# Performance work log

Hardware: AMD Instinct MI355X
Metric: run time of the kernel (lower is better)

## Reference

```python
import math
import jax, jax.numpy as jnp
import numpy as np

B, N, TOKEN_DIM = 8, 8192, 512
NODE_DIM = 64
MAX_NODES = 64
SCORE_HIDDEN = 64


def setup_inputs() -> dict:
    key = jax.random.key(0)
    ks = jax.random.split(key, 8)
    s = lambda k, shape, fan_in: jax.random.normal(k, shape, jnp.float32) / np.sqrt(fan_in)
    return {
        "token_feats": jax.random.normal(ks[0], (B, N, TOKEN_DIM), jnp.float32),
        "score_w1": s(ks[1], (TOKEN_DIM, SCORE_HIDDEN), TOKEN_DIM),
        "score_b1": jnp.zeros((SCORE_HIDDEN,), jnp.float32),
        "score_w2": s(ks[2], (SCORE_HIDDEN, 1), SCORE_HIDDEN),
        "score_b2": jnp.zeros((1,), jnp.float32),
        "t2n_w": s(ks[3], (TOKEN_DIM, NODE_DIM), TOKEN_DIM),
        "n2t_w": s(ks[4], (NODE_DIM, TOKEN_DIM), NODE_DIM),
        "gcn_w1": s(ks[5], (NODE_DIM, NODE_DIM), NODE_DIM),
        "gcn_w2": s(ks[6], (NODE_DIM, NODE_DIM), NODE_DIM),
    }


def reference(token_feats, score_w1, score_b1, score_w2, score_b2,
              t2n_w, n2t_w, gcn_w1, gcn_w2):
    Bn, Nn, d = token_feats.shape
    M = MAX_NODES
    eps = 1e-6

    # --- node selection (scores -> threshold -> top-k among selected) ---
    h = jax.nn.relu(jnp.einsum('bnd,dh->bnh', token_feats, score_w1) + score_b1)
    scores = (jnp.einsum('bnh,ho->bno', h, score_w2) + score_b2)[..., 0]  # [B,N]
    mean = scores.mean(axis=1, keepdims=True)
    std = scores.std(axis=1, keepdims=True)  # unbiased=False (population)
    thr = mean + 0.5 * std
    count = jnp.sum(scores > thr, axis=1)  # [B]
    fallback_k = min(M, max(4, Nn // 16))
    take_k = jnp.where(count == 0, fallback_k, jnp.minimum(count, M))  # [B]

    _, top_idx = jax.lax.top_k(scores, M)  # [B,M] highest scores; set == torch's selection
    node_mask = jnp.arange(M)[None, :] < take_k[:, None]  # [B,M] bool
    maskf = node_mask.astype(token_feats.dtype)

    gathered = jnp.take_along_axis(token_feats, top_idx[..., None], axis=1)  # [B,M,d]
    H0 = jnp.einsum('bmd,dk->bmk', gathered, t2n_w) * maskf[..., None]  # [B,M,node_dim]

    # --- cosine-similarity adjacency, masked, self-loops, row-normalized ---
    nrm = jnp.maximum(jnp.linalg.norm(H0, axis=-1, keepdims=True), eps)
    Hn = H0 / nrm
    A = jax.nn.relu(jnp.einsum('bik,bjk->bij', Hn, Hn))
    A = A * (maskf[:, :, None] * maskf[:, None, :])
    A = A + jnp.eye(M, dtype=A.dtype)[None] * maskf[:, None, :]
    A = A / jnp.maximum(A.sum(axis=-1, keepdims=True), 1e-6)

    # --- two-layer GCN (no bias) ---
    x = jax.nn.relu(jnp.einsum('bij,bjk,kl->bil', A, H0, gcn_w1))
    Hg = jax.nn.relu(jnp.einsum('bij,bjk,kl->bil', A, x, gcn_w2))  # [B,M,node_dim]

    # --- attention scatter-back to tokens ---
    token_proj = jnp.einsum('bnd,dk->bnk', token_feats, t2n_w)  # [B,N,node_dim]
    logits = jnp.einsum('bnk,bmk->bnm', token_proj, Hg) / math.sqrt(NODE_DIM)
    attn = jax.nn.softmax(logits, axis=-1)
    injected = jnp.einsum('bnm,bmk->bnk', attn, Hg)
    back = jnp.einsum('bnk,kd->bnd', injected, n2t_w)
    return token_feats + back
```

## Files before the change

kernel.cpp:

```cpp
#include <hip/hip_runtime.h>
#include <hip/hip_bf16.h>

#define B_ 8
#define N_ 8192
#define D_ 512
#define M_ 64

typedef unsigned short u16;
typedef unsigned int u32;
typedef __attribute__((ext_vector_type(8))) short bf16x8;
typedef __attribute__((ext_vector_type(4))) float f32x4;

__device__ __forceinline__ u16 f2bf(float f) {
  u32 u = __float_as_uint(f);
  u += 0x7FFFu + ((u >> 16) & 1u);
  return (u16)(u >> 16);
}
__device__ __forceinline__ float bf2f(u16 h) {
  return __uint_as_float(((u32)h) << 16);
}

__device__ __forceinline__ int bfrag_idx(int kd, int c, int ncols16) {
  int sub = (kd >> 5) * ncols16 + (c >> 4);
  int lane = (c & 15) + 16 * ((kd & 15) >> 2);
  int e = (kd & 3) + 4 * ((kd >> 4) & 1);
  return sub * 512 + lane * 8 + e;
}

__device__ __forceinline__ int kslot(int ln, int e) {
  return (e & 3) + 4 * (ln >> 4) + 16 * (e >> 2);
}

__device__ __forceinline__ bf16x8 pack8(float4 v0, float4 v1) {
  bf16x8 a;
  a[0] = (short)f2bf(v0.x); a[1] = (short)f2bf(v0.y);
  a[2] = (short)f2bf(v0.z); a[3] = (short)f2bf(v0.w);
  a[4] = (short)f2bf(v1.x); a[5] = (short)f2bf(v1.y);
  a[6] = (short)f2bf(v1.z); a[7] = (short)f2bf(v1.w);
  return a;
}

__global__ __launch_bounds__(256) void k_prep(
    const float* __restrict__ t2n, const float* __restrict__ n2t,
    const float* __restrict__ W1, const float* __restrict__ g1,
    const float* __restrict__ g2,
    u16* __restrict__ t2nf, u16* __restrict__ n2tf,
    u16* __restrict__ W1h, u16* __restrict__ W1l,
    u16* __restrict__ g1f, u16* __restrict__ g2f)
{
  const int gid = blockIdx.x * 256 + threadIdx.x;
  const int stride = gridDim.x * 256;
  for (int s = gid; s < 512 * 64; s += stride) {
    const int k = s >> 6, c = s & 63;
    const int idx = bfrag_idx(k, c, 4);
    t2nf[idx] = f2bf(t2n[s]);
    const float w = W1[s];
    const u16 wh = f2bf(w);
    W1h[idx] = wh;
    W1l[idx] = f2bf(w - bf2f(wh));
  }
  for (int s = gid; s < 64 * 512; s += stride) {
    const int k = s >> 9, c = s & 511;
    n2tf[bfrag_idx(k, c, 32)] = f2bf(n2t[s]);
  }
  for (int s = gid; s < 4096; s += stride) {
    const int k = s >> 6, c = s & 63;
    g1f[bfrag_idx(k, c, 4)] = f2bf(g1[s]);
    g2f[bfrag_idx(k, c, 4)] = f2bf(g2[s]);
  }
}

__global__ __launch_bounds__(256, 4) void k_sp(
    const float* __restrict__ X, const u16* __restrict__ W1h,
    const u16* __restrict__ W1l, const u16* __restrict__ t2nf,
    const float* __restrict__ b1, const float* __restrict__ w2,
    const float* __restrict__ b2, float* __restrict__ scores,
    float* __restrict__ outStash)
{
  __shared__ __align__(16) u16 sB[6144];
  __shared__ __align__(16) u16 sAf[4096];
  const int tid = threadIdx.x;
  const int t0 = blockIdx.x * 64;
  const int wv = tid >> 6, ln = tid & 63;
  const int lq = ln >> 4, lr = ln & 15;
  u16* mySf = &sAf[wv * 1024];
  const float* xr = X + (size_t)(t0 + 16 * wv + lr) * D_;

  f32x4 acc[4], accP[4];
  #pragma unroll
  for (int cb = 0; cb < 4; ++cb) {
    acc[cb] = (f32x4){0.f, 0.f, 0.f, 0.f};
    accP[cb] = (f32x4){0.f, 0.f, 0.f, 0.f};
  }

  auto gsrc = [&](int f, int kb) -> const u16* {
    const int cb = f / 3, mat = f % 3;
    const u16* mp = (mat == 0) ? W1h : (mat == 1) ? W1l : t2nf;
    return mp + (kb * 4 + cb) * 512 + ln * 8;
  };

  bf16x8 wr[3];
  #pragma unroll
  for (int j = 0; j < 3; ++j) wr[j] = *(const bf16x8*)gsrc(j * 4 + wv, 0);
  float4 va0 = *(const float4*)(xr + 4 * lq);
  float4 va1 = *(const float4*)(xr + 16 + 4 * lq);

  for (int kb = 0; kb < 16; ++kb) {
    __syncthreads();
    #pragma unroll
    for (int j = 0; j < 3; ++j)
      *(bf16x8*)&sB[(j * 4 + wv) * 512 + ln * 8] = wr[j];
    __syncthreads();
    const float4 v0 = va0, v1 = va1;
    if (kb < 15) {
      #pragma unroll
      for (int j = 0; j < 3; ++j) wr[j] = *(const bf16x8*)gsrc(j * 4 + wv, kb + 1);
      va0 = *(const float4*)(xr + 32 * (kb + 1) + 4 * lq);
      va1 = *(const float4*)(xr + 32 * (kb + 1) + 16 + 4 * lq);
    }
    const float xs[8] = {v0.x, v0.y, v0.z, v0.w, v1.x, v1.y, v1.z, v1.w};
    bf16x8 ah, al;
    #pragma unroll
    for (int e = 0; e < 8; ++e) {
      const u16 h = f2bf(xs[e]);
      ah[e] = (short)h;
      al[e] = (short)f2bf(xs[e] - bf2f(h));
    }
    #pragma unroll
    for (int cb = 0; cb < 4; ++cb) {
      const bf16x8 bh = *(const bf16x8*)&sB[(cb * 3 + 0) * 512 + ln * 8];
      const bf16x8 bl = *(const bf16x8*)&sB[(cb * 3 + 1) * 512 + ln * 8];
      const bf16x8 bt = *(const bf16x8*)&sB[(cb * 3 + 2) * 512 + ln * 8];
      acc[cb]  = __builtin_amdgcn_mfma_f32_16x16x32_bf16(ah, bh, acc[cb], 0, 0, 0);
      acc[cb]  = __builtin_amdgcn_mfma_f32_16x16x32_bf16(ah, bl, acc[cb], 0, 0, 0);
      acc[cb]  = __builtin_amdgcn_mfma_f32_16x16x32_bf16(al, bh, acc[cb], 0, 0, 0);
      accP[cb] = __builtin_amdgcn_mfma_f32_16x16x32_bf16(ah, bt, accP[cb], 0, 0, 0);
    }
  }

  float b1v[4], w2v[4];
  #pragma unroll
  for (int cb = 0; cb < 4; ++cb) {
    const int col = cb * 16 + lr;
    b1v[cb] = b1[col]; w2v[cb] = w2[col];
  }
  const float b2v = b2[0];
  #pragma unroll
  for (int r = 0; r < 4; ++r) {
    float p = 0.f;
    #pragma unroll
    for (int cb = 0; cb < 4; ++cb) {
      const float h = fmaxf(acc[cb][r] + b1v[cb], 0.f);
      p = fmaf(h, w2v[cb], p);
    }
    p += __shfl_xor(p, 1); p += __shfl_xor(p, 2);
    p += __shfl_xor(p, 4); p += __shfl_xor(p, 8);
    if (lr == 0) scores[t0 + wv * 16 + 4 * lq + r] = p + b2v;
  }

  #pragma unroll
  for (int cb = 0; cb < 4; ++cb)
    #pragma unroll
    for (int r = 0; r < 4; ++r) {
      const int idx = (cb >> 1) * 512 + (4 * lq + r + 16 * (lr >> 2)) * 8 +
                      (lr & 3) + 4 * (cb & 1);
      mySf[idx] = f2bf(accP[cb][r]);
    }
  u16* stash = (u16*)(outStash + (size_t)blockIdx.x * 32768);
  #pragma unroll
  for (int kb2 = 0; kb2 < 2; ++kb2)
    *(bf16x8*)&stash[wv * 1024 + kb2 * 512 + ln * 8] =
        *(const bf16x8*)&mySf[kb2 * 512 + ln * 8];
}

__global__ __launch_bounds__(1024) void k_select(
    const float* __restrict__ scores, int* __restrict__ top_idx,
    int* __restrict__ take_k)
{
  __shared__ float sS[N_];
  __shared__ u32 hist[256];
  __shared__ float redf[34];
  __shared__ u32 redu[16];
  __shared__ u32 sPrefix, sRank, sCntA, sCntT;
  __shared__ int candIdx[64];
  __shared__ float candVal[64];
  __shared__ int tieIdx[128];
  const int b = blockIdx.x, tid = threadIdx.x;
  const int wv = tid >> 6, ln = tid & 63;
  const float* s = scores + (size_t)b * N_;

  float sum = 0.f, sq = 0.f;
  for (int i = tid; i < N_; i += 1024) {
    const float v = s[i]; sS[i] = v; sum += v; sq = fmaf(v, v, sq);
  }
  #pragma unroll
  for (int off = 32; off > 0; off >>= 1) {
    sum += __shfl_xor(sum, off);
    sq  += __shfl_xor(sq, off);
  }
  if (ln == 0) { redf[wv] = sum; redf[16 + wv] = sq; }
  __syncthreads();
  if (tid == 0) {
    float tot = 0.f, totq = 0.f;
    #pragma unroll
    for (int w = 0; w < 16; ++w) { tot += redf[w]; totq += redf[16 + w]; }
    const float mean = tot / (float)N_;
    const float var  = totq / (float)N_ - mean * mean;
    redf[32] = mean + 0.5f * sqrtf(fmaxf(var, 0.f));
  }
  __syncthreads();
  const float thr = redf[32];
  int c = 0;
  for (int i = tid; i < N_; i += 1024) c += (sS[i] > thr) ? 1 : 0;
  #pragma unroll
  for (int off = 32; off > 0; off >>= 1) c += __shfl_xor(c, off);
  if (ln == 0) redu[wv] = (u32)c;
  __syncthreads();
  if (tid == 0) {
    int cnt = 0;
    #pragma unroll
    for (int w = 0; w < 16; ++w) cnt += (int)redu[w];
    take_k[b] = (cnt == 0) ? M_ : (cnt < M_ ? cnt : M_);
  }
  __syncthreads();

  u32 prefix = 0, rank = 64, pmask = 0;
  for (int pass = 0; pass < 4; ++pass) {
    const int shift = 24 - 8 * pass;
    if (tid < 256) hist[tid] = 0;
    __syncthreads();
    for (int i = tid; i < N_; i += 1024) {
      const u32 u = __float_as_uint(sS[i]);
      const u32 key = u ^ ((u32)((int)u >> 31) | 0x80000000u);
      const bool active = (key & pmask) == prefix;
      const int bin = (int)((key >> shift) & 255u);
      if (pass == 0) {
        unsigned long long act = __ballot(active);
        while (act) {
          const int leader = (int)__builtin_ctzll(act);
          const int lbin = __shfl(bin, leader);
          const unsigned long long eq = __ballot(active && (bin == lbin));
          if (ln == leader) atomicAdd(&hist[lbin], (u32)__builtin_popcountll(eq));
          act &= ~eq;
        }
      } else {
        if (active) atomicAdd(&hist[bin], 1u);
      }
    }
    __syncthreads();
    if (tid < 64) {
      const u32 h0 = hist[4 * tid], h1 = hist[4 * tid + 1];
      const u32 h2 = hist[4 * tid + 2], h3 = hist[4 * tid + 3];
      const u32 s3 = h3, s2 = h2 + s3, s1 = h1 + s2, s0 = h0 + s1;
      u32 run = s0;
      #pragma unroll
      for (int off = 1; off < 64; off <<= 1) {
        const u32 t = (u32)__shfl_down((int)run, off);
        if (tid + off < 64) run += t;
      }
      const u32 excl = run - s0;
      const u32 c0 = s0 + excl, c1 = s1 + excl, c2 = s2 + excl, c3 = s3 + excl;
      int pick = -1; u32 nxt = 0;
      if (c0 >= rank && c1 < rank)        { pick = 0; nxt = c1; }
      else if (c1 >= rank && c2 < rank)   { pick = 1; nxt = c2; }
      else if (c2 >= rank && c3 < rank)   { pick = 2; nxt = c3; }
      else if (c3 >= rank && excl < rank) { pick = 3; nxt = excl; }
      if (pick >= 0) {
        sPrefix = prefix | ((u32)(4 * tid + pick) << shift);
        sRank = rank - nxt;
      }
    }
    __syncthreads();
    prefix = sPrefix; rank = sRank;
    pmask |= 0xFFu << shift;
    __syncthreads();
  }

  if (tid == 0) { sCntA = 0; sCntT = 0; }
  __syncthreads();
  const u32 pivot = prefix;
  for (int i = tid; i < N_; i += 1024) {
    const u32 u = __float_as_uint(sS[i]);
    const u32 key = u ^ ((u32)((int)u >> 31) | 0x80000000u);
    if (key > pivot) {
      const u32 p = atomicAdd(&sCntA, 1u);
      candIdx[p] = i; candVal[p] = sS[i];
    } else if (key == pivot) {
      const u32 p = atomicAdd(&sCntT, 1u);
      if (p < 128) tieIdx[p] = i;
    }
  }
  __syncthreads();
  if (tid == 0) {
    const int nA = (int)sCntA;
    const int need = 64 - nA;
    int nT = (int)sCntT; if (nT > 128) nT = 128;
    for (int j = 0; j < need; ++j) {
      int bi = 1 << 30, bp = -1;
      for (int q = 0; q < nT; ++q) {
        const int v = tieIdx[q];
        if (v >= 0 && v < bi) { bi = v; bp = q; }
      }
      candIdx[nA + j] = bi; candVal[nA + j] = sS[bi]; tieIdx[bp] = -1;
    }
  }
  __syncthreads();
  if (tid < 64) {
    const float v = candVal[tid]; const int ii = candIdx[tid];
    int rk = 0;
    for (int j = 0; j < 64; ++j) {
      const float vj = candVal[j]; const int ij = candIdx[j];
      rk += (vj > v || (vj == v && ij < ii)) ? 1 : 0;
    }
    top_idx[b * M_ + rk] = ii;
  }
}

__device__ __forceinline__ bf16x8 ldsA_frag(const float (*S)[65], int wv, int kb, int ln) {
  const int lr = ln & 15;
  bf16x8 a;
  #pragma unroll
  for (int e = 0; e < 8; ++e) a[e] = (short)f2bf(S[16 * wv + lr][32 * kb + kslot(ln, e)]);
  return a;
}
__device__ __forceinline__ bf16x8 ldsB_frag(const float (*S)[65], int cb, int kb, int ln) {
  const int lr = ln & 15;
  bf16x8 bb;
  #pragma unroll
  for (int e = 0; e < 8; ++e) bb[e] = (short)f2bf(S[32 * kb + kslot(ln, e)][16 * cb + lr]);
  return bb;
}
__device__ __forceinline__ bf16x8 ldsBT_frag(const float (*S)[65], int cb, int kb, int ln) {
  const int lr = ln & 15;
  bf16x8 bb;
  #pragma unroll
  for (int e = 0; e < 8; ++e) bb[e] = (short)f2bf(S[16 * cb + lr][32 * kb + kslot(ln, e)]);
  return bb;
}

__global__ __launch_bounds__(256) void k_graph(
    const float* __restrict__ X, const u16* __restrict__ t2nf,
    const u16* __restrict__ n2tf, const u16* __restrict__ g1f,
    const u16* __restrict__ g2f, const int* __restrict__ top_idx,
    const int* __restrict__ take_k, u16* __restrict__ HgTf,
    u16* __restrict__ Wf)
{
  __shared__ float sH0[64][65];
  __shared__ float sA[64][65];
  __shared__ float sT[64][65];
  __shared__ float sU[64][65];
  __shared__ float sR[64];
  const int b = blockIdx.x, tid = threadIdx.x;
  const int wv = tid >> 6, ln = tid & 63;
  const int lq = ln >> 4, lr = ln & 15;
  const int tk = take_k[b];
  const int rowm = 16 * wv + 4 * lq;

  const int gidx = top_idx[b * M_ + 16 * wv + lr];
  const float* xr = X + ((size_t)b * N_ + gidx) * D_;
  f32x4 d[4];
  #pragma unroll
  for (int cb = 0; cb < 4; ++cb) d[cb] = (f32x4){0.f, 0.f, 0.f, 0.f};
  {
    float4 p0[3], p1[3];
    #pragma unroll
    for (int q = 0; q < 3; ++q) {
      p0[q] = *(const float4*)(xr + 32 * q + 4 * lq);
      p1[q] = *(const float4*)(xr + 32 * q + 16 + 4 * lq);
    }
    #pragma unroll
    for (int kb = 0; kb < 16; ++kb) {
      const int slot = kb % 3;
      const float4 v0 = p0[slot], v1 = p1[slot];
      if (kb + 3 < 16) {
        p0[slot] = *(const float4*)(xr + 32 * (kb + 3) + 4 * lq);
        p1[slot] = *(const float4*)(xr + 32 * (kb + 3) + 16 + 4 * lq);
      }
      const bf16x8 a = pack8(v0, v1);
      #pragma unroll
      for (int cb = 0; cb < 4; ++cb) {
        const bf16x8 bb = *(const bf16x8*)&t2nf[(kb * 4 + cb) * 512 + ln * 8];
        d[cb] = __builtin_amdgcn_mfma_f32_16x16x32_bf16(a, bb, d[cb], 0, 0, 0);
      }
    }
  }
  #pragma unroll
  for (int cb = 0; cb < 4; ++cb)
    #pragma unroll
    for (int r = 0; r < 4; ++r)
      sH0[rowm + r][16 * cb + lr] = (rowm + r < tk) ? d[cb][r] : 0.f;
  __syncthreads();

  if (tid < 64) {
    float s = 0.f;
    #pragma unroll
    for (int k = 0; k < 64; ++k) { const float v = sH0[tid][k]; s = fmaf(v, v, s); }
    sR[tid] = 1.f / fmaxf(sqrtf(s), 1e-6f);
  }
  __syncthreads();
  #pragma unroll
  for (int p = 0; p < 16; ++p) {
    const int o = tid + p * 256;
    const int i = o >> 6, k = o & 63;
    sU[i][k] = sH0[i][k] * sR[i];
  }
  __syncthreads();

  #pragma unroll
  for (int cb = 0; cb < 4; ++cb) d[cb] = (f32x4){0.f, 0.f, 0.f, 0.f};
  #pragma unroll
  for (int kb = 0; kb < 2; ++kb) {
    const bf16x8 a = ldsA_frag(sU, wv, kb, ln);
    #pragma unroll
    for (int cb = 0; cb < 4; ++cb)
      d[cb] = __builtin_amdgcn_mfma_f32_16x16x32_bf16(a, ldsBT_frag(sU, cb, kb, ln), d[cb], 0, 0, 0);
  }
  __syncthreads();
  #pragma unroll
  for (int cb = 0; cb < 4; ++cb)
    #pragma unroll
    for (int r = 0; r < 4; ++r) {
      const int row = rowm + r, col = 16 * cb + lr;
      float s = fmaxf(d[cb][r], 0.f);
      s = (row < tk && col < tk) ? s : 0.f;
      if (row == col && row < tk) s += 1.f;
      sA[row][col] = s;
    }
  __syncthreads();

  if (tid < 64) {
    float rs = 0.f;
    #pragma unroll
    for (int j = 0; j < 64; ++j) rs += sA[tid][j];
    sR[tid] = 1.f / fmaxf(rs, 1e-6f);
  }
  __syncthreads();
  #pragma unroll
  for (int p = 0; p < 16; ++p) {
    const int o = tid + p * 256;
    const int i = o >> 6, j = o & 63;
    sA[i][j] *= sR[i];
  }
  __syncthreads();

  #pragma unroll
  for (int cb = 0; cb < 4; ++cb) d[cb] = (f32x4){0.f, 0.f, 0.f, 0.f};
  #pragma unroll
  for (int kb = 0; kb < 2; ++kb) {
    const bf16x8 a = ldsA_frag(sA, wv, kb, ln);
    #pragma unroll
    for (int cb = 0; cb < 4; ++cb)
      d[cb] = __builtin_amdgcn_mfma_f32_16x16x32_bf16(a, ldsB_frag(sH0, cb, kb, ln), d[cb], 0, 0, 0);
  }
  __syncthreads();
  #pragma unroll
  for (int cb = 0; cb < 4; ++cb)
    #pragma unroll
    for (int r = 0; r < 4; ++r) sT[rowm + r][16 * cb + lr] = d[cb][r];
  __syncthreads();

  #pragma unroll
  for (int cb = 0; cb < 4; ++cb) d[cb] = (f32x4){0.f, 0.f, 0.f, 0.f};
  #pragma unroll
  for (int kb = 0; kb < 2; ++kb) {
    const bf16x8 a = ldsA_frag(sT, wv, kb, ln);
    #pragma unroll
    for (int cb = 0; cb < 4; ++cb) {
      const bf16x8 bb = *(const bf16x8*)&g1f[(kb * 4 + cb) * 512 + ln * 8];
      d[cb] = __builtin_amdgcn_mfma_f32_16x16x32_bf16(a, bb, d[cb], 0, 0, 0);
    }
  }
  __syncthreads();
  #pragma unroll
  for (int cb = 0; cb < 4; ++cb)
    #pragma unroll
    for (int r = 0; r < 4; ++r) sU[rowm + r][16 * cb + lr] = fmaxf(d[cb][r], 0.f);
  __syncthreads();

  #pragma unroll
  for (int cb = 0; cb < 4; ++cb) d[cb] = (f32x4){0.f, 0.f, 0.f, 0.f};
  #pragma unroll
  for (int kb = 0; kb < 2; ++kb) {
    const bf16x8 a = ldsA_frag(sA, wv, kb, ln);
    #pragma unroll
    for (int cb = 0; cb < 4; ++cb)
      d[cb] = __builtin_amdgcn_mfma_f32_16x16x32_bf16(a, ldsB_frag(sU, cb, kb, ln), d[cb], 0, 0, 0);
  }
  __syncthreads();
  #pragma unroll
  for (int cb = 0; cb < 4; ++cb)
    #pragma unroll
    for (int r = 0; r < 4; ++r) sT[rowm + r][16 * cb + lr] = d[cb][r];
  __syncthreads();

  #pragma unroll
  for (int cb = 0; cb < 4; ++cb) d[cb] = (f32x4){0.f, 0.f, 0.f, 0.f};
  #pragma unroll
  for (int kb = 0; kb < 2; ++kb) {
    const bf16x8 a = ldsA_frag(sT, wv, kb, ln);
    #pragma unroll
    for (int cb = 0; cb < 4; ++cb) {
      const bf16x8 bb = *(const bf16x8*)&g2f[(kb * 4 + cb) * 512 + ln * 8];
      d[cb] = __builtin_amdgcn_mfma_f32_16x16x32_bf16(a, bb, d[cb], 0, 0, 0);
    }
  }
  __syncthreads();
  #pragma unroll
  for (int cb = 0; cb < 4; ++cb)
    #pragma unroll
    for (int r = 0; r < 4; ++r) {
      const int node = rowm + r, feat = 16 * cb + lr;
      const float hv = fmaxf(d[cb][r], 0.f);
      HgTf[(size_t)b * 4096 + bfrag_idx(feat, node, 4)] = f2bf(hv);
      sU[node][feat] = hv;
    }
  __syncthreads();

  for (int chk = 0; chk < 4; ++chk) {
    f32x4 aw[8];
    #pragma unroll
    for (int c8 = 0; c8 < 8; ++c8) aw[c8] = (f32x4){0.f, 0.f, 0.f, 0.f};
    #pragma unroll
    for (int kbf = 0; kbf < 2; ++kbf) {
      const bf16x8 a = ldsA_frag(sU, wv, kbf, ln);
      #pragma unroll
      for (int c8 = 0; c8 < 8; ++c8) {
        const bf16x8 bb = *(const bf16x8*)&n2tf[(kbf * 32 + chk * 8 + c8) * 512 + ln * 8];
        aw[c8] = __builtin_amdgcn_mfma_f32_16x16x32_bf16(a, bb, aw[c8], 0, 0, 0);
      }
    }
    #pragma unroll
    for (int c8 = 0; c8 < 8; ++c8)
      #pragma unroll
      for (int r = 0; r < 4; ++r) {
        const int m = 16 * wv + 4 * lq + r;
        const int c = (chk * 8 + c8) * 16 + lr;
        Wf[(size_t)b * 32768 + bfrag_idx(m, c, 32)] = f2bf(aw[c8][r]);
      }
  }
}

__global__ __launch_bounds__(256) void k_attn(
    const float* __restrict__ X, const u16* __restrict__ HgTf,
    const u16* __restrict__ Wf, float* __restrict__ out)
{
  __shared__ __align__(16) u16 sAf[4096];
  __shared__ __align__(16) float sBo[4][16][68];
  const int tid = threadIdx.x;
  const int b = blockIdx.x >> 7;
  const int t0 = (blockIdx.x & 127) << 6;
  const float* Xb = X + (size_t)b * N_ * D_;
  float* Ob = out + (size_t)b * N_ * D_;
  const int wv = tid >> 6, ln = tid & 63;
  const int lq = ln >> 4, lr = ln & 15;
  u16* mySf = &sAf[wv * 1024];
  const u16* stash = (const u16*)(out + (size_t)blockIdx.x * 32768);

  f32x4 accL[4];
  #pragma unroll
  for (int cb = 0; cb < 4; ++cb) accL[cb] = (f32x4){0.f, 0.f, 0.f, 0.f};
  #pragma unroll
  for (int kb = 0; kb < 2; ++kb) {
    const bf16x8 a = *(const bf16x8*)&stash[wv * 1024 + kb * 512 + ln * 8];
    #pragma unroll
    for (int cb = 0; cb < 4; ++cb) {
      const bf16x8 bb = *(const bf16x8*)&HgTf[(size_t)b * 4096 + (kb * 4 + cb) * 512 + ln * 8];
      accL[cb] = __builtin_amdgcn_mfma_f32_16x16x32_bf16(a, bb, accL[cb], 0, 0, 0);
    }
  }
  __syncthreads();

  float attnv[4][4];
  #pragma unroll
  for (int r = 0; r < 4; ++r) {
    const float v0 = accL[0][r], v1 = accL[1][r], v2 = accL[2][r], v3 = accL[3][r];
    float mx = fmaxf(fmaxf(v0, v1), fmaxf(v2, v3));
    mx = fmaxf(mx, __shfl_xor(mx, 1)); mx = fmaxf(mx, __shfl_xor(mx, 2));
    mx = fmaxf(mx, __shfl_xor(mx, 4)); mx = fmaxf(mx, __shfl_xor(mx, 8));
    const float e0 = __expf((v0 - mx) * 0.125f), e1 = __expf((v1 - mx) * 0.125f);
    const float e2 = __expf((v2 - mx) * 0.125f), e3 = __expf((v3 - mx) * 0.125f);
    float sm = (e0 + e1) + (e2 + e3);
    sm += __shfl_xor(sm, 1); sm += __shfl_xor(sm, 2);
    sm += __shfl_xor(sm, 4); sm += __shfl_xor(sm, 8);
    const float inv = 1.f / sm;
    attnv[0][r] = e0 * inv; attnv[1][r] = e1 * inv;
    attnv[2][r] = e2 * inv; attnv[3][r] = e3 * inv;
  }
  #pragma unroll
  for (int cb = 0; cb < 4; ++cb)
    #pragma unroll
    for (int r = 0; r < 4; ++r) {
      const int idx = (cb >> 1) * 512 + (4 * lq + r + 16 * (lr >> 2)) * 8 +
                      (lr & 3) + 4 * (cb & 1);
      mySf[idx] = f2bf(attnv[cb][r]);
    }

  for (int chk = 0; chk < 4; ++chk) {
    float4 xres[8];
    #pragma unroll
    for (int h = 0; h < 2; ++h)
      #pragma unroll
      for (int j = 0; j < 4; ++j)
        xres[h * 4 + j] = *(const float4*)(
            Xb + (size_t)(t0 + 16 * wv + 4 * j + lq) * D_ + chk * 128 + h * 64 + 4 * lr);

    f32x4 accB[8];
    #pragma unroll
    for (int c8 = 0; c8 < 8; ++c8) accB[c8] = (f32x4){0.f, 0.f, 0.f, 0.f};
    #pragma unroll
    for (int kb = 0; kb < 2; ++kb) {
      const bf16x8 a = *(const bf16x8*)&mySf[kb * 512 + ln * 8];
      #pragma unroll
      for (int c8 = 0; c8 < 8; ++c8) {
        const bf16x8 bb = *(const bf16x8*)&Wf[(size_t)b * 32768 + (kb * 32 + chk * 8 + c8) * 512 + ln * 8];
        accB[c8] = __builtin_amdgcn_mfma_f32_16x16x32_bf16(a, bb, accB[c8], 0, 0, 0);
      }
    }
    #pragma unroll
    for (int h = 0; h < 2; ++h) {
      #pragma unroll
      for (int c4 = 0; c4 < 4; ++c4)
        #pragma unroll
        for (int r = 0; r < 4; ++r)
          sBo[wv][4 * lq + r][c4 * 16 + lr] = accB[4 * h + c4][r];
      #pragma unroll
      for (int j = 0; j < 4; ++j) {
        const int rloc = 4 * j + lq;
        float4 v = *(const float4*)&sBo[wv][rloc][4 * lr];
        const float4 xv = xres[h * 4 + j];
        v.x += xv.x; v.y += xv.y; v.z += xv.z; v.w += xv.w;
        *(float4*)(Ob + (size_t)(t0 + 16 * wv + rloc) * D_ + chk * 128 + h * 64 + 4 * lr) = v;
      }
    }
  }
}

extern "C" void kernel_launch(void* const* d_in, const int* in_sizes, int n_in,
                              void* d_out, int out_size, void* d_ws, size_t ws_size,
                              hipStream_t stream)
{
  (void)in_sizes; (void)n_in; (void)out_size; (void)ws_size;
  const float* X   = (const float*)d_in[0];
  const float* W1  = (const float*)d_in[1];
  const float* b1  = (const float*)d_in[2];
  const float* w2  = (const float*)d_in[3];
  const float* b2  = (const float*)d_in[4];
  const float* t2n = (const float*)d_in[5];
  const float* n2t = (const float*)d_in[6];
  const float* g1  = (const float*)d_in[7];
  const float* g2  = (const float*)d_in[8];
  float* out = (float*)d_out;

  char* ws = (char*)d_ws;
  float* scores = (float*)(ws);
  u16* t2nf     = (u16*)(ws + 262144);
  u16* n2tf     = (u16*)(ws + 327680);
  u16* W1h      = (u16*)(ws + 393216);
  u16* W1l      = (u16*)(ws + 458752);
  u16* HgTf     = (u16*)(ws + 524288);
  u16* g1f      = (u16*)(ws + 589824);
  u16* g2f      = (u16*)(ws + 598016);
  int* top_idx  = (int*)(ws + 606208);
  int* take_k   = (int*)(ws + 608256);
  u16* Wf       = (u16*)(ws + 609280);

  k_prep<<<64, 256, 0, stream>>>(t2n, n2t, W1, g1, g2, t2nf, n2tf, W1h, W1l, g1f, g2f);
  k_sp<<<1024, 256, 0, stream>>>(X, W1h, W1l, t2nf, b1, w2, b2, scores, out);
  k_select<<<B_, 1024, 0, stream>>>(scores, top_idx, take_k);
  k_graph<<<B_, 256, 0, stream>>>(X, t2nf, n2tf, g1f, g2f, top_idx, take_k, HgTf, Wf);
  k_attn<<<1024, 256, 0, stream>>>(X, HgTf, Wf, out);
}
```

Baseline: 132.3 us.

## Double-buffer weight tiles in k_sp and keep scores in registers in k_select

In the score/projection kernel, the shared weight tile is now double-buffered: the next k-block is written to the other buffer while MFMAs read the current one. This drops one of the two barriers per iteration and prefetches two blocks ahead. Separately, the selection kernel keeps each thread's 8 scores and radix keys in registers instead of an 8192-float shared array. It builds the first histogram pass during the count loop and uses wave shuffles for the small final reductions. The cost is more LDS in k_sp (possible occupancy impact at 4 blocks/CU) and more registers in k_select; the pass-0 ballot aggregation is replaced by plain atomics.

```diff
diff --git a/kernel.cpp b/kernel.cpp
--- a/kernel.cpp
+++ b/kernel.cpp
@@ -77,7 +77,7 @@
     const float* __restrict__ b2, float* __restrict__ scores,
     float* __restrict__ outStash)
 {
-  __shared__ __align__(16) u16 sB[6144];
+  __shared__ __align__(16) u16 sB[2][6144];
   __shared__ __align__(16) u16 sAf[4096];
   const int tid = threadIdx.x;
   const int t0 = blockIdx.x * 64;
@@ -101,20 +101,27 @@
 
   bf16x8 wr[3];
   #pragma unroll
-  for (int j = 0; j < 3; ++j) wr[j] = *(const bf16x8*)gsrc(j * 4 + wv, 0);
+  for (int j = 0; j < 3; ++j)
+    *(bf16x8*)&sB[0][(j * 4 + wv) * 512 + ln * 8] = *(const bf16x8*)gsrc(j * 4 + wv, 0);
+  #pragma unroll
+  for (int j = 0; j < 3; ++j) wr[j] = *(const bf16x8*)gsrc(j * 4 + wv, 1);
   float4 va0 = *(const float4*)(xr + 4 * lq);
   float4 va1 = *(const float4*)(xr + 16 + 4 * lq);
+  __syncthreads();
 
   for (int kb = 0; kb < 16; ++kb) {
-    __syncthreads();
-    #pragma unroll
-    for (int j = 0; j < 3; ++j)
-      *(bf16x8*)&sB[(j * 4 + wv) * 512 + ln * 8] = wr[j];
-    __syncthreads();
+    const int cur = kb & 1;
+    if (kb < 15) {
+      #pragma unroll
+      for (int j = 0; j < 3; ++j)
+        *(bf16x8*)&sB[cur ^ 1][(j * 4 + wv) * 512 + ln * 8] = wr[j];
+    }
+    if (kb < 14) {
+      #pragma unroll
+      for (int j = 0; j < 3; ++j) wr[j] = *(const bf16x8*)gsrc(j * 4 + wv, kb + 2);
+    }
     const float4 v0 = va0, v1 = va1;
     if (kb < 15) {
-      #pragma unroll
-      for (int j = 0; j < 3; ++j) wr[j] = *(const bf16x8*)gsrc(j * 4 + wv, kb + 1);
       va0 = *(const float4*)(xr + 32 * (kb + 1) + 4 * lq);
       va1 = *(const float4*)(xr + 32 * (kb + 1) + 16 + 4 * lq);
     }
@@ -128,14 +135,15 @@
     }
     #pragma unroll
     for (int cb = 0; cb < 4; ++cb) {
-      const bf16x8 bh = *(const bf16x8*)&sB[(cb * 3 + 0) * 512 + ln * 8];
-      const bf16x8 bl = *(const bf16x8*)&sB[(cb * 3 + 1) * 512 + ln * 8];
-      const bf16x8 bt = *(const bf16x8*)&sB[(cb * 3 + 2) * 512 + ln * 8];
+      const bf16x8 bh = *(const bf16x8*)&sB[cur][(cb * 3 + 0) * 512 + ln * 8];
+      const bf16x8 bl = *(const bf16x8*)&sB[cur][(cb * 3 + 1) * 512 + ln * 8];
+      const bf16x8 bt = *(const bf16x8*)&sB[cur][(cb * 3 + 2) * 512 + ln * 8];
       acc[cb]  = __builtin_amdgcn_mfma_f32_16x16x32_bf16(ah, bh, acc[cb], 0, 0, 0);
       acc[cb]  = __builtin_amdgcn_mfma_f32_16x16x32_bf16(ah, bl, acc[cb], 0, 0, 0);
       acc[cb]  = __builtin_amdgcn_mfma_f32_16x16x32_bf16(al, bh, acc[cb], 0, 0, 0);
       accP[cb] = __builtin_amdgcn_mfma_f32_16x16x32_bf16(ah, bt, accP[cb], 0, 0, 0);
     }
+    __syncthreads();
   }
 
   float b1v[4], w2v[4];
@@ -177,7 +185,6 @@
     const float* __restrict__ scores, int* __restrict__ top_idx,
     int* __restrict__ take_k)
 {
-  __shared__ float sS[N_];
   __shared__ u32 hist[256];
   __shared__ float redf[34];
   __shared__ u32 redu[16];
@@ -189,10 +196,16 @@
   const int wv = tid >> 6, ln = tid & 63;
   const float* s = scores + (size_t)b * N_;
 
+  float v[8]; u32 key[8];
   float sum = 0.f, sq = 0.f;
-  for (int i = tid; i < N_; i += 1024) {
-    const float v = s[i]; sS[i] = v; sum += v; sq = fmaf(v, v, sq);
-  }
+  #pragma unroll
+  for (int j = 0; j < 8; ++j) {
+    v[j] = s[tid + j * 1024];
+    sum += v[j]; sq = fmaf(v[j], v[j], sq);
+    const u32 u = __float_as_uint(v[j]);
+    key[j] = u ^ ((u32)((int)u >> 31) | 0x80000000u);
+  }
+  if (tid < 256) hist[tid] = 0;
   #pragma unroll
   for (int off = 32; off > 0; off >>= 1) {
     sum += __shfl_xor(sum, off);
@@ -200,54 +213,53 @@
   }
   if (ln == 0) { redf[wv] = sum; redf[16 + wv] = sq; }
   __syncthreads();
-  if (tid == 0) {
-    float tot = 0.f, totq = 0.f;
-    #pragma unroll
-    for (int w = 0; w < 16; ++w) { tot += redf[w]; totq += redf[16 + w]; }
-    const float mean = tot / (float)N_;
-    const float var  = totq / (float)N_ - mean * mean;
-    redf[32] = mean + 0.5f * sqrtf(fmaxf(var, 0.f));
+  if (tid < 16) {
+    float a = redf[tid], q = redf[16 + tid];
+    #pragma unroll
+    for (int off = 8; off > 0; off >>= 1) {
+      a += __shfl_down(a, off);
+      q += __shfl_down(q, off);
+    }
+    if (tid == 0) {
+      const float mean = a / (float)N_;
+      const float var = q / (float)N_ - mean * mean;
+      redf[32] = mean + 0.5f * sqrtf(fmaxf(var, 0.f));
+    }
   }
   __syncthreads();
   const float thr = redf[32];
+
   int c = 0;
-  for (int i = tid; i < N_; i += 1024) c += (sS[i] > thr) ? 1 : 0;
+  #pragma unroll
+  for (int j = 0; j < 8; ++j) {
+    c += (v[j] > thr) ? 1 : 0;
+    atomicAdd(&hist[key[j] >> 24], 1u);
+  }
   #pragma unroll
   for (int off = 32; off > 0; off >>= 1) c += __shfl_xor(c, off);
   if (ln == 0) redu[wv] = (u32)c;
   __syncthreads();
-  if (tid == 0) {
-    int cnt = 0;
-    #pragma unroll
-    for (int w = 0; w < 16; ++w) cnt += (int)redu[w];
-    take_k[b] = (cnt == 0) ? M_ : (cnt < M_ ? cnt : M_);
-  }
-  __syncthreads();
+  if (tid < 16) {
+    u32 a = redu[tid];
+    #pragma unroll
+    for (int off = 8; off > 0; off >>= 1) a += (u32)__shfl_down((int)a, off);
+    if (tid == 0) {
+      const int cnt = (int)a;
+      take_k[b] = (cnt == 0) ? M_ : (cnt < M_ ? cnt : M_);
+    }
+  }
 
   u32 prefix = 0, rank = 64, pmask = 0;
   for (int pass = 0; pass < 4; ++pass) {
     const int shift = 24 - 8 * pass;
-    if (tid < 256) hist[tid] = 0;
-    __syncthreads();
-    for (int i = tid; i < N_; i += 1024) {
-      const u32 u = __float_as_uint(sS[i]);
-      const u32 key = u ^ ((u32)((int)u >> 31) | 0x80000000u);
-      const bool active = (key & pmask) == prefix;
-      const int bin = (int)((key >> shift) & 255u);
-      if (pass == 0) {
-        unsigned long long act = __ballot(active);
-        while (act) {
-          const int leader = (int)__builtin_ctzll(act);
-          const int lbin = __shfl(bin, leader);
-          const unsigned long long eq = __ballot(active && (bin == lbin));
-          if (ln == leader) atomicAdd(&hist[lbin], (u32)__builtin_popcountll(eq));
-          act &= ~eq;
-        }
-      } else {
-        if (active) atomicAdd(&hist[bin], 1u);
-      }
-    }
-    __syncthreads();
+    if (pass > 0) {
+      if (tid < 256) hist[tid] = 0;
+      __syncthreads();
+      #pragma unroll
+      for (int j = 0; j < 8; ++j)
+        if ((key[j] & pmask) == prefix) atomicAdd(&hist[(key[j] >> shift) & 255u], 1u);
+      __syncthreads();
+    }
     if (tid < 64) {
       const u32 h0 = hist[4 * tid], h1 = hist[4 * tid + 1];
       const u32 h2 = hist[4 * tid + 2], h3 = hist[4 * tid + 3];
@@ -279,15 +291,14 @@
   if (tid == 0) { sCntA = 0; sCntT = 0; }
   __syncthreads();
   const u32 pivot = prefix;
-  for (int i = tid; i < N_; i += 1024) {
-    const u32 u = __float_as_uint(sS[i]);
-    const u32 key = u ^ ((u32)((int)u >> 31) | 0x80000000u);
-    if (key > pivot) {
+  #pragma unroll
+  for (int j = 0; j < 8; ++j) {
+    if (key[j] > pivot) {
       const u32 p = atomicAdd(&sCntA, 1u);
-      candIdx[p] = i; candVal[p] = sS[i];
-    } else if (key == pivot) {
+      candIdx[p] = tid + j * 1024; candVal[p] = v[j];
+    } else if (key[j] == pivot) {
       const u32 p = atomicAdd(&sCntT, 1u);
-      if (p < 128) tieIdx[p] = i;
+      if (p < 128) tieIdx[p] = tid + j * 1024;
     }
   }
   __syncthreads();
@@ -295,22 +306,25 @@
     const int nA = (int)sCntA;
     const int need = 64 - nA;
     int nT = (int)sCntT; if (nT > 128) nT = 128;
+    const float pv = (pivot & 0x80000000u)
+                         ? __uint_as_float(pivot ^ 0x80000000u)
+                         : __uint_as_float(~pivot);
     for (int j = 0; j < need; ++j) {
       int bi = 1 << 30, bp = -1;
       for (int q = 0; q < nT; ++q) {
-        const int v = tieIdx[q];
-        if (v >= 0 && v < bi) { bi = v; bp = q; }
-      }
-      candIdx[nA + j] = bi; candVal[nA + j] = sS[bi]; tieIdx[bp] = -1;
+        const int vv = tieIdx[q];
+        if (vv >= 0 && vv < bi) { bi = vv; bp = q; }
+      }
+      candIdx[nA + j] = bi; candVal[nA + j] = pv; tieIdx[bp] = -1;
     }
   }
   __syncthreads();
   if (tid < 64) {
-    const float v = candVal[tid]; const int ii = candIdx[tid];
+    const float vv = candVal[tid]; const int ii = candIdx[tid];
     int rk = 0;
     for (int j = 0; j < 64; ++j) {
       const float vj = candVal[j]; const int ij = candIdx[j];
-      rk += (vj > v || (vj == v && ij < ii)) ? 1 : 0;
+      rk += (vj > vv || (vj == vv && ij < ii)) ? 1 : 0;
     }
     top_idx[b * M_ + rk] = ii;
   }
@@ -392,17 +406,16 @@
   __syncthreads();
 
   if (tid < 64) {
-    float s = 0.f;
-    #pragma unroll
-    for (int k = 0; k < 64; ++k) { const float v = sH0[tid][k]; s = fmaf(v, v, s); }
-    sR[tid] = 1.f / fmaxf(sqrtf(s), 1e-6f);
+    float ss = 0.f;
+    #pragma unroll
+    for (int k = 0; k < 64; ++k) { const float vv = sH0[tid][k]; ss = fmaf(vv, vv, ss); }
+    sR[tid] = 1.f / fmaxf(sqrtf(ss), 1e-6f);
   }
   __syncthreads();
   #pragma unroll
   for (int p = 0; p < 16; ++p) {
     const int o = tid + p * 256;
-    const int i = o >> 6, k = o & 63;
-    sU[i][k] = sH0[i][k] * sR[i];
+    sU[o >> 6][o & 63] = sH0[o >> 6][o & 63] * sR[o >> 6];
   }
   __syncthreads();
 
@@ -421,10 +434,10 @@
     #pragma unroll
     for (int r = 0; r < 4; ++r) {
       const int row = rowm + r, col = 16 * cb + lr;
-      float s = fmaxf(d[cb][r], 0.f);
-      s = (row < tk && col < tk) ? s : 0.f;
-      if (row == col && row < tk) s += 1.f;
-      sA[row][col] = s;
+      float ss = fmaxf(d[cb][r], 0.f);
+      ss = (row < tk && col < tk) ? ss : 0.f;
+      if (row == col && row < tk) ss += 1.f;
+      sA[row][col] = ss;
     }
   __syncthreads();
 
@@ -438,8 +451,7 @@
   #pragma unroll
   for (int p = 0; p < 16; ++p) {
     const int o = tid + p * 256;
-    const int i = o >> 6, j = o & 63;
-    sA[i][j] *= sR[i];
+    sA[o >> 6][o & 63] *= sR[o >> 6];
   }
   __syncthreads();
 
@@ -534,8 +546,8 @@
       #pragma unroll
       for (int r = 0; r < 4; ++r) {
         const int m = 16 * wv + 4 * lq + r;
-        const int c = (chk * 8 + c8) * 16 + lr;
-        Wf[(size_t)b * 32768 + bfrag_idx(m, c, 32)] = f2bf(aw[c8][r]);
+        const int cc = (chk * 8 + c8) * 16 + lr;
+        Wf[(size_t)b * 32768 + bfrag_idx(m, cc, 32)] = f2bf(aw[c8][r]);
       }
   }
 }
@@ -626,10 +638,10 @@
       #pragma unroll
       for (int j = 0; j < 4; ++j) {
         const int rloc = 4 * j + lq;
-        float4 v = *(const float4*)&sBo[wv][rloc][4 * lr];
+        float4 vv = *(const float4*)&sBo[wv][rloc][4 * lr];
         const float4 xv = xres[h * 4 + j];
-        v.x += xv.x; v.y += xv.y; v.z += xv.z; v.w += xv.w;
-        *(float4*)(Ob + (size_t)(t0 + 16 * wv + rloc) * D_ + chk * 128 + h * 64 + 4 * lr) = v;
+        vv.x += xv.x; vv.y += xv.y; vv.z += xv.z; vv.w += xv.w;
+        *(float4*)(Ob + (size_t)(t0 + 16 * wv + rloc) * D_ + chk * 128 + h * 64 + 4 * lr) = vv;
       }
     }
   }
```

Result: faster. 127.8 us (-3.4%).
